# Kernel tuning notes

Measured on AMD Instinct MI355X. Metric: run time of the kernel, lower is better.

Reference implementation:

```python
import jax, jax.numpy as jnp
import numpy as np

D_MODEL = 1024
HEAD_SIZE = 64

def setup_inputs() -> dict:
    key = jax.random.key(0)
    ks = jax.random.split(key, 7)
    s = 1.0 / np.sqrt(D_MODEL)
    return {
        "x": jax.random.normal(ks[0], (4, 2048, D_MODEL), dtype=jnp.float32),
        "wq": jax.random.uniform(ks[1], (D_MODEL, HEAD_SIZE), jnp.float32, -s, s),
        "bq": jax.random.uniform(ks[2], (HEAD_SIZE,), jnp.float32, -s, s),
        "wk": jax.random.uniform(ks[3], (D_MODEL, HEAD_SIZE), jnp.float32, -s, s),
        "bk": jax.random.uniform(ks[4], (HEAD_SIZE,), jnp.float32, -s, s),
        "wv": jax.random.uniform(ks[5], (D_MODEL, HEAD_SIZE), jnp.float32, -s, s),
        "bv": jax.random.uniform(ks[6], (HEAD_SIZE,), jnp.float32, -s, s),
    }

def reference(x, wq, bq, wk, bk, wv, bv):
    # x: [b, n, d_model]; projections -> [b, n, head_size]
    q = x @ wq + bq
    k = x @ wk + bk
    v = x @ wv + bv
    scores = jnp.einsum("bnd,bmd->bnm", q, k) / jnp.sqrt(jnp.float32(HEAD_SIZE))
    attn = jax.nn.softmax(scores, axis=-1)  # [b, n, n]
    return jnp.einsum("bnm,bmd->bnd", attn, v)
```

## Files before the change

### kernel.cpp

```cpp
#include <hip/hip_runtime.h>
#include <math.h>

#define D_MODEL 1024
#define HEAD 64
#define SEQ 2048
#define BATCH 4

typedef _Float16 f16x4 __attribute__((ext_vector_type(4)));
typedef _Float16 f16x8 __attribute__((ext_vector_type(8)));
typedef float f32x4 __attribute__((ext_vector_type(4)));

__global__ __launch_bounds__(256) void prep_w(
    const float* __restrict__ wq, const float* __restrict__ wk,
    const float* __restrict__ wv, _Float16* __restrict__ wT)
{
    const float* w = (blockIdx.y == 0) ? wq : (blockIdx.y == 1) ? wk : wv;
    const int kbase = blockIdx.x * 64;
    __shared__ float t[64][65];
    const int tid = threadIdx.x;
    #pragma unroll
    for (int i = 0; i < 16; i++) {
        int idx = tid + i * 256;
        int kk = idx >> 6, c = idx & 63;
        t[kk][c] = w[(size_t)(kbase + kk) * 64 + c];
    }
    __syncthreads();
    #pragma unroll
    for (int i = 0; i < 16; i++) {
        int idx = tid + i * 256;
        int c = idx >> 6, kk = idx & 63;
        wT[(size_t)(blockIdx.y * 64 + c) * 1024 + kbase + kk] = (_Float16)t[kk][c];
    }
}

__global__ __launch_bounds__(768, 6) void proj_kernel(
    const float* __restrict__ x, const _Float16* __restrict__ wT,
    const float* __restrict__ bq, const float* __restrict__ bk2,
    const float* __restrict__ bv,
    _Float16* __restrict__ q, _Float16* __restrict__ k, _Float16* __restrict__ vT)
{
    const int tid = threadIdx.x;
    const int wave = tid >> 6;
    const int lane = tid & 63;
    const int l16 = lane & 15;
    const int quad = lane >> 4;
    const int row0 = blockIdx.x * 16;

    __shared__ __align__(16) _Float16 Xs[2][16][136];

    const int srow = tid >> 5;
    const int sc4 = tid & 31;
    const float4* xg = reinterpret_cast<const float4*>(x)
                     + (size_t)(row0 + srow) * (D_MODEL / 4) + sc4;

    const _Float16* wp = wT + (size_t)(wave * 16 + l16) * D_MODEL + quad * 8;

    float4 xr;
    if (tid < 512) {
        xr = xg[0];
        f16x4 h;
        h[0] = (_Float16)xr.x; h[1] = (_Float16)xr.y;
        h[2] = (_Float16)xr.z; h[3] = (_Float16)xr.w;
        *(f16x4*)&Xs[0][srow][sc4 * 4] = h;
    }

    f32x4 acc = (f32x4){0.f, 0.f, 0.f, 0.f};

    #pragma unroll 1
    for (int c = 0; c < 8; c++) {
        __syncthreads();
        f16x8 bw0 = *(const f16x8*)(wp + c * 128);
        f16x8 bw1 = *(const f16x8*)(wp + c * 128 + 32);
        f16x8 bw2 = *(const f16x8*)(wp + c * 128 + 64);
        f16x8 bw3 = *(const f16x8*)(wp + c * 128 + 96);
        if (c < 7 && tid < 512) xr = xg[(c + 1) * 32];
        const int bsel = c & 1;
        f16x8 aX0 = *(const f16x8*)&Xs[bsel][l16][0 * 32 + quad * 8];
        f16x8 aX1 = *(const f16x8*)&Xs[bsel][l16][1 * 32 + quad * 8];
        f16x8 aX2 = *(const f16x8*)&Xs[bsel][l16][2 * 32 + quad * 8];
        f16x8 aX3 = *(const f16x8*)&Xs[bsel][l16][3 * 32 + quad * 8];
        acc = __builtin_amdgcn_mfma_f32_16x16x32_f16(aX0, bw0, acc, 0, 0, 0);
        acc = __builtin_amdgcn_mfma_f32_16x16x32_f16(aX1, bw1, acc, 0, 0, 0);
        acc = __builtin_amdgcn_mfma_f32_16x16x32_f16(aX2, bw2, acc, 0, 0, 0);
        acc = __builtin_amdgcn_mfma_f32_16x16x32_f16(aX3, bw3, acc, 0, 0, 0);
        if (c < 7 && tid < 512) {
            f16x4 h;
            h[0] = (_Float16)xr.x; h[1] = (_Float16)xr.y;
            h[2] = (_Float16)xr.z; h[3] = (_Float16)xr.w;
            *(f16x4*)&Xs[bsel ^ 1][srow][sc4 * 4] = h;
        }
    }

    const int g = wave * 16 + l16;
    const int batch = row0 / SEQ;
    const int rbase = row0 + quad * 4;
    if (g < 64) {
        float bias = bq[g];
        #pragma unroll
        for (int r = 0; r < 4; r++)
            q[(size_t)(rbase + r) * HEAD + g] = (_Float16)((acc[r] + bias) * 0.125f);
    } else if (g < 128) {
        float bias = bk2[g - 64];
        #pragma unroll
        for (int r = 0; r < 4; r++)
            k[(size_t)(rbase + r) * HEAD + (g - 64)] = (_Float16)(acc[r] + bias);
    } else {
        float bias = bv[g - 128];
        f16x4 pk;
        #pragma unroll
        for (int r = 0; r < 4; r++) pk[r] = (_Float16)(acc[r] + bias);
        const int seq0 = row0 - batch * SEQ + quad * 4;
        const int d = g - 128;
        *(f16x4*)(vT + ((size_t)(batch * 128 + (seq0 >> 4)) * 64 + d) * 16 + (seq0 & 15)) = pk;
    }
}

__global__ __launch_bounds__(512) void attn_kernel(
    const _Float16* __restrict__ q, const _Float16* __restrict__ k,
    const _Float16* __restrict__ vT, float* __restrict__ out)
{
    const int tid = threadIdx.x;
    const int wave = tid >> 6;
    const int lane = tid & 63;
    const int l16 = lane & 15;
    const int quad = lane >> 4;
    const int b = blockIdx.y;
    const int q0 = blockIdx.x * 32;

    __shared__ __align__(16) char SM[69632];
    _Float16* KV = (_Float16*)SM;
    float (*Oall)[2][16][68] = (float(*)[2][16][68])SM;
    __shared__ float Lall[8][2][16];

    const int wb = wave * 4096;

    f16x8 bQ00, bQ01, bQ10, bQ11;
    {
        const _Float16* qp = q + (size_t)(b * SEQ + q0 + l16) * HEAD + quad * 8;
        bQ00 = *(const f16x8*)qp;
        bQ01 = *(const f16x8*)(qp + 32);
        bQ10 = *(const f16x8*)(qp + 16 * HEAD);
        bQ11 = *(const f16x8*)(qp + 16 * HEAD + 32);
    }

    const _Float16* kgb = k + (size_t)(b * SEQ + wave * 256) * HEAD + lane * 8;
    const _Float16* vgb = vT + (size_t)(b * 128 + wave * 16) * 1024 + lane * 8;

    const int kw = (lane >> 3) * 64 + (((lane & 7) ^ (lane >> 3)) * 8);
    const int vw = lane * 8;

    f32x4 O0[4], O1[4];
    #pragma unroll
    for (int dt = 0; dt < 4; dt++) {
        O0[dt] = (f32x4){0.f, 0.f, 0.f, 0.f};
        O1[dt] = (f32x4){0.f, 0.f, 0.f, 0.f};
    }
    float lp0 = 0.f, lp1 = 0.f;

    f16x8 kr0[3], kr1[3], vr0[3], vr1[3];

#define LOADS(SI, STRIP) { \
        kr0[SI] = *(const f16x8*)(kgb + (STRIP) * 1024); \
        kr1[SI] = *(const f16x8*)(kgb + (STRIP) * 1024 + 512); \
        vr0[SI] = *(const f16x8*)(vgb + (STRIP) * 1024); \
        vr1[SI] = *(const f16x8*)(vgb + (STRIP) * 1024 + 512); \
    }

#define WRITES(SI, NSEL) { \
        *(f16x8*)&KV[wb + (NSEL) * 1024 + kw] = kr0[SI]; \
        *(f16x8*)&KV[wb + (NSEL) * 1024 + kw + 512] = kr1[SI]; \
        *(f16x8*)&KV[wb + 2048 + (NSEL) * 1024 + vw] = vr0[SI]; \
        *(f16x8*)&KV[wb + 2048 + (NSEL) * 1024 + vw + 512] = vr1[SI]; \
    }

#define COMP(BSEL) { \
        const _Float16* Kl = KV + wb + (BSEL) * 1024; \
        const _Float16* Vl = KV + wb + 2048 + (BSEL) * 1024; \
        f16x8 aK0 = *(const f16x8*)&Kl[l16 * 64 + ((quad ^ (l16 & 7)) * 8)]; \
        f16x8 aK1 = *(const f16x8*)&Kl[l16 * 64 + (((quad + 4) ^ (l16 & 7)) * 8)]; \
        f32x4 s0 = __builtin_amdgcn_mfma_f32_16x16x32_f16(aK0, bQ00, (f32x4){0.f, 0.f, 0.f, 0.f}, 0, 0, 0); \
        s0 = __builtin_amdgcn_mfma_f32_16x16x32_f16(aK1, bQ01, s0, 0, 0, 0); \
        f32x4 s1 = __builtin_amdgcn_mfma_f32_16x16x32_f16(aK0, bQ10, (f32x4){0.f, 0.f, 0.f, 0.f}, 0, 0, 0); \
        s1 = __builtin_amdgcn_mfma_f32_16x16x32_f16(aK1, bQ11, s1, 0, 0, 0); \
        float p00 = __expf(s0[0]), p01 = __expf(s0[1]); \
        float p02 = __expf(s0[2]), p03 = __expf(s0[3]); \
        float p10 = __expf(s1[0]), p11 = __expf(s1[1]); \
        float p12 = __expf(s1[2]), p13 = __expf(s1[3]); \
        lp0 += (p00 + p01) + (p02 + p03); \
        lp1 += (p10 + p11) + (p12 + p13); \
        f16x4 bP0, bP1; \
        bP0[0] = (_Float16)p00; bP0[1] = (_Float16)p01; \
        bP0[2] = (_Float16)p02; bP0[3] = (_Float16)p03; \
        bP1[0] = (_Float16)p10; bP1[1] = (_Float16)p11; \
        bP1[2] = (_Float16)p12; bP1[3] = (_Float16)p13; \
        _Pragma("unroll") \
        for (int dt = 0; dt < 4; dt++) { \
            f16x4 aV = *(const f16x4*)&Vl[(dt * 16 + l16) * 16 + quad * 4]; \
            O0[dt] = __builtin_amdgcn_mfma_f32_16x16x16f16(aV, bP0, O0[dt], 0, 0, 0); \
            O1[dt] = __builtin_amdgcn_mfma_f32_16x16x16f16(aV, bP1, O1[dt], 0, 0, 0); \
        } \
    }

#define ITER(C) { \
        if ((C) <= 12) LOADS(((C) + 3) % 3, (C) + 3) \
        COMP((C) & 1) \
        if ((C) <= 14) WRITES(((C) + 1) % 3, ((C) + 1) & 1) \
    }

    LOADS(0, 0)
    LOADS(1, 1)
    LOADS(2, 2)
    WRITES(0, 0)

    ITER(0)  ITER(1)  ITER(2)  ITER(3)
    ITER(4)  ITER(5)  ITER(6)  ITER(7)
    ITER(8)  ITER(9)  ITER(10) ITER(11)
    ITER(12) ITER(13) ITER(14) ITER(15)

#undef LOADS
#undef WRITES
#undef COMP
#undef ITER

    lp0 += __shfl_xor(lp0, 16);
    lp0 += __shfl_xor(lp0, 32);
    lp1 += __shfl_xor(lp1, 16);
    lp1 += __shfl_xor(lp1, 32);
    __syncthreads();
    if (lane < 16) {
        Lall[wave][0][l16] = lp0;
        Lall[wave][1][l16] = lp1;
    }
    #pragma unroll
    for (int dt = 0; dt < 4; dt++) {
        *(f32x4*)&Oall[wave][0][l16][dt * 16 + quad * 4] = O0[dt];
        *(f32x4*)&Oall[wave][1][l16][dt * 16 + quad * 4] = O1[dt];
    }
    __syncthreads();

    {
        int qi = tid >> 4;
        int dd = (tid & 15) * 4;
        int t = qi >> 4, q16 = qi & 15;
        float L = 0.f, a0 = 0.f, a1 = 0.f, a2 = 0.f, a3 = 0.f;
        #pragma unroll
        for (int w = 0; w < 8; w++) {
            L += Lall[w][t][q16];
            const float* op = &Oall[w][t][q16][dd];
            a0 += op[0]; a1 += op[1]; a2 += op[2]; a3 += op[3];
        }
        float inv = 1.f / L;
        float4 res = make_float4(a0 * inv, a1 * inv, a2 * inv, a3 * inv);
        *(float4*)(out + (size_t)(b * SEQ + q0 + qi) * HEAD + dd) = res;
    }
}

extern "C" void kernel_launch(void* const* d_in, const int* in_sizes, int n_in,
                              void* d_out, int out_size, void* d_ws, size_t ws_size,
                              hipStream_t stream) {
    const float* x  = (const float*)d_in[0];
    const float* wq = (const float*)d_in[1];
    const float* bq = (const float*)d_in[2];
    const float* wk = (const float*)d_in[3];
    const float* bk = (const float*)d_in[4];
    const float* wv = (const float*)d_in[5];
    const float* bv = (const float*)d_in[6];
    float* out = (float*)d_out;

    const size_t proj_elems = (size_t)BATCH * SEQ * HEAD;
    _Float16* qh = (_Float16*)d_ws;
    _Float16* kh = qh + proj_elems;
    _Float16* vT = kh + proj_elems;
    _Float16* wT = vT + proj_elems;

    prep_w<<<dim3(16, 3), 256, 0, stream>>>(wq, wk, wv, wT);
    proj_kernel<<<dim3(BATCH * SEQ / 16), 768, 0, stream>>>(x, wT, bq, bk, bv, qh, kh, vT);
    attn_kernel<<<dim3(SEQ / 32, BATCH), 512, 0, stream>>>(qh, kh, vT, out);
}
```

Measured before the change: 116.9 us.

## Store K and V in MFMA fragment order and load them directly into registers

The projection kernel now writes K and V in a layout that matches the per-lane MFMA operand fragments. The attention kernel can then read operands straight from global memory into registers, with no staging through shared memory, a 4-deep register prefetch, and one fewer barrier. This removes the LDS write/read traffic and the staging stores from the attention loop. In exchange it relies on the L2 cache for K/V reuse across blocks, uses more registers, and the K stores in projection become scattered 2-byte writes.

```diff
diff --git a/kernel.cpp b/kernel.cpp
--- a/kernel.cpp
+++ b/kernel.cpp
@@ -37,7 +37,7 @@
     const float* __restrict__ x, const _Float16* __restrict__ wT,
     const float* __restrict__ bq, const float* __restrict__ bk2,
     const float* __restrict__ bv,
-    _Float16* __restrict__ q, _Float16* __restrict__ k, _Float16* __restrict__ vT)
+    _Float16* __restrict__ q, _Float16* __restrict__ kF, _Float16* __restrict__ vF)
 {
     const int tid = threadIdx.x;
     const int wave = tid >> 6;
@@ -94,30 +94,37 @@
     const int g = wave * 16 + l16;
     const int batch = row0 / SEQ;
     const int rbase = row0 + quad * 4;
+    const int seq0 = row0 - batch * SEQ + quad * 4;
     if (g < 64) {
         float bias = bq[g];
         #pragma unroll
         for (int r = 0; r < 4; r++)
             q[(size_t)(rbase + r) * HEAD + g] = (_Float16)((acc[r] + bias) * 0.125f);
     } else if (g < 128) {
-        float bias = bk2[g - 64];
+        const int d = g - 64;
+        float bias = bk2[d];
+        _Float16* kp = kF + (size_t)batch * (SEQ * HEAD)
+                     + (size_t)(((seq0 >> 4) * 2 + (d >> 5)) * 64
+                                + (seq0 & 15) + 16 * ((d >> 3) & 3)) * 8 + (d & 7);
         #pragma unroll
         for (int r = 0; r < 4; r++)
-            k[(size_t)(rbase + r) * HEAD + (g - 64)] = (_Float16)(acc[r] + bias);
+            kp[r * 8] = (_Float16)(acc[r] + bias);
     } else {
-        float bias = bv[g - 128];
+        const int d = g - 128;
+        float bias = bv[d];
         f16x4 pk;
         #pragma unroll
         for (int r = 0; r < 4; r++) pk[r] = (_Float16)(acc[r] + bias);
-        const int seq0 = row0 - batch * SEQ + quad * 4;
-        const int d = g - 128;
-        *(f16x4*)(vT + ((size_t)(batch * 128 + (seq0 >> 4)) * 64 + d) * 16 + (seq0 & 15)) = pk;
+        _Float16* vp = vF + (size_t)batch * (SEQ * HEAD)
+                     + (size_t)(((seq0 >> 4) * 4 + (d >> 4)) * 64
+                                + (d & 15) + 16 * quad) * 4;
+        *(f16x4*)vp = pk;
     }
 }
 
 __global__ __launch_bounds__(512) void attn_kernel(
-    const _Float16* __restrict__ q, const _Float16* __restrict__ k,
-    const _Float16* __restrict__ vT, float* __restrict__ out)
+    const _Float16* __restrict__ q, const _Float16* __restrict__ kF,
+    const _Float16* __restrict__ vF, float* __restrict__ out)
 {
     const int tid = threadIdx.x;
     const int wave = tid >> 6;
@@ -127,12 +134,8 @@
     const int b = blockIdx.y;
     const int q0 = blockIdx.x * 32;
 
-    __shared__ __align__(16) char SM[69632];
-    _Float16* KV = (_Float16*)SM;
-    float (*Oall)[2][16][68] = (float(*)[2][16][68])SM;
+    __shared__ __align__(16) float Oall[8][2][16][68];
     __shared__ float Lall[8][2][16];
-
-    const int wb = wave * 4096;
 
     f16x8 bQ00, bQ01, bQ10, bQ11;
     {
@@ -143,11 +146,8 @@
         bQ11 = *(const f16x8*)(qp + 16 * HEAD + 32);
     }
 
-    const _Float16* kgb = k + (size_t)(b * SEQ + wave * 256) * HEAD + lane * 8;
-    const _Float16* vgb = vT + (size_t)(b * 128 + wave * 16) * 1024 + lane * 8;
-
-    const int kw = (lane >> 3) * 64 + (((lane & 7) ^ (lane >> 3)) * 8);
-    const int vw = lane * 8;
+    const _Float16* kgb = kF + (size_t)b * (SEQ * HEAD) + wave * 16 * 1024 + lane * 8;
+    const _Float16* vgb = vF + (size_t)b * (SEQ * HEAD) + wave * 16 * 1024 + lane * 4;
 
     f32x4 O0[4], O1[4];
     #pragma unroll
@@ -157,31 +157,23 @@
     }
     float lp0 = 0.f, lp1 = 0.f;
 
-    f16x8 kr0[3], kr1[3], vr0[3], vr1[3];
+    f16x8 kr0[4], kr1[4];
+    f16x4 vv0[4], vv1[4], vv2[4], vv3[4];
 
 #define LOADS(SI, STRIP) { \
         kr0[SI] = *(const f16x8*)(kgb + (STRIP) * 1024); \
         kr1[SI] = *(const f16x8*)(kgb + (STRIP) * 1024 + 512); \
-        vr0[SI] = *(const f16x8*)(vgb + (STRIP) * 1024); \
-        vr1[SI] = *(const f16x8*)(vgb + (STRIP) * 1024 + 512); \
-    }
-
-#define WRITES(SI, NSEL) { \
-        *(f16x8*)&KV[wb + (NSEL) * 1024 + kw] = kr0[SI]; \
-        *(f16x8*)&KV[wb + (NSEL) * 1024 + kw + 512] = kr1[SI]; \
-        *(f16x8*)&KV[wb + 2048 + (NSEL) * 1024 + vw] = vr0[SI]; \
-        *(f16x8*)&KV[wb + 2048 + (NSEL) * 1024 + vw + 512] = vr1[SI]; \
-    }
-
-#define COMP(BSEL) { \
-        const _Float16* Kl = KV + wb + (BSEL) * 1024; \
-        const _Float16* Vl = KV + wb + 2048 + (BSEL) * 1024; \
-        f16x8 aK0 = *(const f16x8*)&Kl[l16 * 64 + ((quad ^ (l16 & 7)) * 8)]; \
-        f16x8 aK1 = *(const f16x8*)&Kl[l16 * 64 + (((quad + 4) ^ (l16 & 7)) * 8)]; \
-        f32x4 s0 = __builtin_amdgcn_mfma_f32_16x16x32_f16(aK0, bQ00, (f32x4){0.f, 0.f, 0.f, 0.f}, 0, 0, 0); \
-        s0 = __builtin_amdgcn_mfma_f32_16x16x32_f16(aK1, bQ01, s0, 0, 0, 0); \
-        f32x4 s1 = __builtin_amdgcn_mfma_f32_16x16x32_f16(aK0, bQ10, (f32x4){0.f, 0.f, 0.f, 0.f}, 0, 0, 0); \
-        s1 = __builtin_amdgcn_mfma_f32_16x16x32_f16(aK1, bQ11, s1, 0, 0, 0); \
+        vv0[SI] = *(const f16x4*)(vgb + (STRIP) * 1024); \
+        vv1[SI] = *(const f16x4*)(vgb + (STRIP) * 1024 + 256); \
+        vv2[SI] = *(const f16x4*)(vgb + (STRIP) * 1024 + 512); \
+        vv3[SI] = *(const f16x4*)(vgb + (STRIP) * 1024 + 768); \
+    }
+
+#define COMP(SI) { \
+        f32x4 s0 = __builtin_amdgcn_mfma_f32_16x16x32_f16(kr0[SI], bQ00, (f32x4){0.f, 0.f, 0.f, 0.f}, 0, 0, 0); \
+        s0 = __builtin_amdgcn_mfma_f32_16x16x32_f16(kr1[SI], bQ01, s0, 0, 0, 0); \
+        f32x4 s1 = __builtin_amdgcn_mfma_f32_16x16x32_f16(kr0[SI], bQ10, (f32x4){0.f, 0.f, 0.f, 0.f}, 0, 0, 0); \
+        s1 = __builtin_amdgcn_mfma_f32_16x16x32_f16(kr1[SI], bQ11, s1, 0, 0, 0); \
         float p00 = __expf(s0[0]), p01 = __expf(s0[1]); \
         float p02 = __expf(s0[2]), p03 = __expf(s0[3]); \
         float p10 = __expf(s1[0]), p11 = __expf(s1[1]); \
@@ -193,24 +185,22 @@
         bP0[2] = (_Float16)p02; bP0[3] = (_Float16)p03; \
         bP1[0] = (_Float16)p10; bP1[1] = (_Float16)p11; \
         bP1[2] = (_Float16)p12; bP1[3] = (_Float16)p13; \
-        _Pragma("unroll") \
-        for (int dt = 0; dt < 4; dt++) { \
-            f16x4 aV = *(const f16x4*)&Vl[(dt * 16 + l16) * 16 + quad * 4]; \
-            O0[dt] = __builtin_amdgcn_mfma_f32_16x16x16f16(aV, bP0, O0[dt], 0, 0, 0); \
-            O1[dt] = __builtin_amdgcn_mfma_f32_16x16x16f16(aV, bP1, O1[dt], 0, 0, 0); \
-        } \
+        O0[0] = __builtin_amdgcn_mfma_f32_16x16x16f16(vv0[SI], bP0, O0[0], 0, 0, 0); \
+        O1[0] = __builtin_amdgcn_mfma_f32_16x16x16f16(vv0[SI], bP1, O1[0], 0, 0, 0); \
+        O0[1] = __builtin_amdgcn_mfma_f32_16x16x16f16(vv1[SI], bP0, O0[1], 0, 0, 0); \
+        O1[1] = __builtin_amdgcn_mfma_f32_16x16x16f16(vv1[SI], bP1, O1[1], 0, 0, 0); \
+        O0[2] = __builtin_amdgcn_mfma_f32_16x16x16f16(vv2[SI], bP0, O0[2], 0, 0, 0); \
+        O1[2] = __builtin_amdgcn_mfma_f32_16x16x16f16(vv2[SI], bP1, O1[2], 0, 0, 0); \
+        O0[3] = __builtin_amdgcn_mfma_f32_16x16x16f16(vv3[SI], bP0, O0[3], 0, 0, 0); \
+        O1[3] = __builtin_amdgcn_mfma_f32_16x16x16f16(vv3[SI], bP1, O1[3], 0, 0, 0); \
     }
 
 #define ITER(C) { \
-        if ((C) <= 12) LOADS(((C) + 3) % 3, (C) + 3) \
-        COMP((C) & 1) \
-        if ((C) <= 14) WRITES(((C) + 1) % 3, ((C) + 1) & 1) \
-    }
-
-    LOADS(0, 0)
-    LOADS(1, 1)
-    LOADS(2, 2)
-    WRITES(0, 0)
+        COMP((C) & 3) \
+        if ((C) <= 11) LOADS((C) & 3, (C) + 4) \
+    }
+
+    LOADS(0, 0) LOADS(1, 1) LOADS(2, 2) LOADS(3, 3)
 
     ITER(0)  ITER(1)  ITER(2)  ITER(3)
     ITER(4)  ITER(5)  ITER(6)  ITER(7)
@@ -218,7 +208,6 @@
     ITER(12) ITER(13) ITER(14) ITER(15)
 
 #undef LOADS
-#undef WRITES
 #undef COMP
 #undef ITER
 
@@ -226,7 +215,6 @@
     lp0 += __shfl_xor(lp0, 32);
     lp1 += __shfl_xor(lp1, 16);
     lp1 += __shfl_xor(lp1, 32);
-    __syncthreads();
     if (lane < 16) {
         Lall[wave][0][l16] = lp0;
         Lall[wave][1][l16] = lp1;
@@ -269,11 +257,11 @@
 
     const size_t proj_elems = (size_t)BATCH * SEQ * HEAD;
     _Float16* qh = (_Float16*)d_ws;
-    _Float16* kh = qh + proj_elems;
-    _Float16* vT = kh + proj_elems;
-    _Float16* wT = vT + proj_elems;
+    _Float16* kFh = qh + proj_elems;
+    _Float16* vFh = kFh + proj_elems;
+    _Float16* wT = vFh + proj_elems;
 
     prep_w<<<dim3(16, 3), 256, 0, stream>>>(wq, wk, wv, wT);
-    proj_kernel<<<dim3(BATCH * SEQ / 16), 768, 0, stream>>>(x, wT, bq, bk, bv, qh, kh, vT);
-    attn_kernel<<<dim3(SEQ / 32, BATCH), 512, 0, stream>>>(qh, kh, vT, out);
-}
+    proj_kernel<<<dim3(BATCH * SEQ / 16), 768, 0, stream>>>(x, wT, bq, bk, bv, qh, kFh, vFh);
+    attn_kernel<<<dim3(SEQ / 32, BATCH), 512, 0, stream>>>(qh, kFh, vFh, out);
+}
```

Measured after the change: 115.7 us. About the same (-1.1%).
